# Kernel tuning notes

Measured on AMD Instinct MI355X. Metric: run time of the kernel, lower is better.

## Reference

```python
import jax, jax.numpy as jnp
import numpy as np

D, H, N, BS = 3072, 2048, 16, 512
MAX_LATENT_VAR = 0.1


def setup_inputs() -> dict:
    key = jax.random.key(0)
    ks = jax.random.split(key, 12)
    s = 0.02
    return {
        "x": jax.random.normal(ks[0], (BS, D), dtype=jnp.float32),
        "eps": jax.random.normal(ks[1], (1, BS, N), dtype=jnp.float32),
        "enc_W1": jax.random.normal(ks[2], (D, H), dtype=jnp.float32) * s,
        "enc_b1": jnp.zeros((H,), dtype=jnp.float32),
        "enc_Wmu": jax.random.normal(ks[3], (H, N), dtype=jnp.float32) * s,
        "enc_bmu": jnp.zeros((N,), dtype=jnp.float32),
        "enc_Wls": jax.random.normal(ks[4], (H, 1), dtype=jnp.float32) * s,
        "enc_bls": jnp.zeros((1,), dtype=jnp.float32),
        "dec_W1": jax.random.normal(ks[5], (N, H), dtype=jnp.float32) * 0.1,
        "dec_b1": jnp.zeros((H,), dtype=jnp.float32),
        "dec_W2": jax.random.normal(ks[6], (H, D), dtype=jnp.float32) * s,
        "dec_b2": jnp.zeros((D,), dtype=jnp.float32),
    }


def reference(x, eps, enc_W1, enc_b1, enc_Wmu, enc_bmu, enc_Wls, enc_bls,
              dec_W1, dec_b1, dec_W2, dec_b2):
    bs, Dd = x.shape
    n = dec_W1.shape[0]

    def dec(z):  # smooth 2-layer MLP decoder (supports nested autodiff)
        return jnp.tanh(z @ dec_W1 + dec_b1) @ dec_W2 + dec_b2

    # encoder.forward_with_sigma
    h = jnp.tanh(x @ enc_W1 + enc_b1)
    z_star = h @ enc_Wmu + enc_bmu                      # (bs, n)
    sigma = jnp.exp(h @ enc_Wls + enc_bls)[:, 0]        # (bs,)

    # per-sample Jacobian of decoder: (bs, D, n)
    J = jax.vmap(jax.jacfwd(dec))(z_star)

    # per-sample Hessian of f(z) = stop_grad(d) . d,  d = (x - dec(z)) / sigma
    def f_hess(z, xi, sg):
        d = (xi - dec(z)) / sg
        return jnp.dot(jax.lax.stop_gradient(d), d)
    hess = jax.vmap(jax.hessian(f_hess), in_axes=(0, 0, 0))(z_star, x, sigma)  # (bs,n,n)

    eye = jnp.eye(n, dtype=x.dtype)
    Prec = jnp.einsum('bdi,bdj->bij', J, J) / (sigma ** 2)[:, None, None] + eye + hess

    eigvals = jnp.linalg.eigvalsh(Prec)                 # ascending, (bs, n)
    eigmin = eigvals[:, 0]
    delta = 1.0 / MAX_LATENT_VAR - eigmin               # (bs,)
    Prec = Prec + eye * delta[:, None, None]
    eigvals = eigvals + delta[:, None]

    # upper-triangular Cholesky: U^T U = Prec
    U = jnp.swapaxes(jnp.linalg.cholesky(Prec), -1, -2)  # (bs, n, n)

    def solve1(u, e):  # solve U y = e
        return jax.scipy.linalg.solve_triangular(u, e[:, None], lower=False)[:, 0]
    z_off = jax.vmap(jax.vmap(solve1, in_axes=(0, 0)), in_axes=(None, 0))(U, eps)  # (ne,bs,n)
    z_sample = z_star[None] + z_off

    n_eval = eps.shape[0]
    recon = dec(z_sample.reshape(-1, n)).reshape(n_eval, bs, Dd)
    recon_loss = ((recon - x[None]) ** 2).sum(axis=2).mean(axis=0) / (2.0 * sigma ** 2)
    latent_energy = (z_star ** 2).sum(axis=1) / 2.0 + (1.0 / eigvals).sum(axis=1) / 2.0
    logdet_loss = jnp.log(eigvals).sum(axis=1) / 2.0
    sigma_loss = Dd * jnp.log(sigma)
    neg_log_prob = (recon_loss + latent_energy + logdet_loss + sigma_loss) / Dd
    return (neg_log_prob, recon_loss, latent_energy, logdet_loss, sigma)
```

## Files before the change

kernel.cpp:

```cpp
#include <hip/hip_runtime.h>
#include <hip/hip_bf16.h>
#include <math.h>

#define D_ 3072
#define H_ 2048
#define N_ 16
#define BS_ 512
#define NSL_ 8

typedef short s16x8 __attribute__((ext_vector_type(8)));
typedef float f32x4v __attribute__((ext_vector_type(4)));
typedef __hip_bfloat16 bf16;

__device__ __forceinline__ void gload_lds16(const void* g, void* l) {
    __builtin_amdgcn_global_load_lds((const __attribute__((address_space(1))) void*)g,
                                     (__attribute__((address_space(3))) void*)l, 16, 0, 0);
}

__device__ __forceinline__ float bf2f(unsigned short u) {
    unsigned v = (unsigned)u << 16; float f; __builtin_memcpy(&f, &v, 4); return f;
}

__global__ __launch_bounds__(256) void mfma_nt_slab(
    const bf16* __restrict__ A, const bf16* __restrict__ Bt,
    float* __restrict__ C, int M, int N, int K, int KC)
{
    __shared__ __align__(16) bf16 As[128 * 32];
    __shared__ __align__(16) bf16 Bs[128 * 32];
    const int tid = threadIdx.x;
    const int w = tid >> 6, l = tid & 63;
    const int wr = w >> 1, wc = w & 1;
    const int m0 = blockIdx.y * 128, n0 = blockIdx.x * 128;
    const int kbeg = blockIdx.z * KC;
    float* Cz = C + (size_t)blockIdx.z * M * N;

    f32x4v acc[4][4];
    #pragma unroll
    for (int a = 0; a < 4; ++a)
        #pragma unroll
        for (int b = 0; b < 4; ++b) acc[a][b] = (f32x4v){0.f, 0.f, 0.f, 0.f};

    const int srow = l >> 2;
    const int scol = (l & 3) * 8;

    for (int k0 = kbeg; k0 < kbeg + KC; k0 += 32) {
        #pragma unroll
        for (int q = 0; q < 2; ++q) {
            int r0 = w * 32 + q * 16;
            gload_lds16(&A[(size_t)(m0 + r0 + srow) * K + k0 + scol], &As[r0 * 32]);
            gload_lds16(&Bt[(size_t)(n0 + r0 + srow) * K + k0 + scol], &Bs[r0 * 32]);
        }
        __syncthreads();
        s16x8 af[4], bfr[4];
        #pragma unroll
        for (int mf = 0; mf < 4; ++mf)
            af[mf] = *(const s16x8*)&As[(wr * 64 + mf * 16 + (l & 15)) * 32 + (l >> 4) * 8];
        #pragma unroll
        for (int nf = 0; nf < 4; ++nf)
            bfr[nf] = *(const s16x8*)&Bs[(wc * 64 + nf * 16 + (l & 15)) * 32 + (l >> 4) * 8];
        #pragma unroll
        for (int mf = 0; mf < 4; ++mf)
            #pragma unroll
            for (int nf = 0; nf < 4; ++nf)
                acc[mf][nf] = __builtin_amdgcn_mfma_f32_16x16x32_bf16(af[mf], bfr[nf], acc[mf][nf], 0, 0, 0);
        __syncthreads();
    }

    #pragma unroll
    for (int mf = 0; mf < 4; ++mf)
        #pragma unroll
        for (int nf = 0; nf < 4; ++nf) {
            int n = n0 + wc * 64 + nf * 16 + (l & 15);
            #pragma unroll
            for (int r = 0; r < 4; ++r) {
                int m = m0 + wr * 64 + mf * 16 + (l >> 4) * 4 + r;
                Cz[(size_t)m * N + n] = acc[mf][nf][r];
            }
        }
}

__global__ __launch_bounds__(256) void mfma_nt_sk(
    const bf16* __restrict__ A, const bf16* __restrict__ Bt,
    float* __restrict__ C, int M, int N, int K, int KC)
{
    __shared__ __align__(16) bf16 As[128 * 32];
    __shared__ __align__(16) bf16 Bs[128 * 32];
    const int tid = threadIdx.x;
    const int w = tid >> 6, l = tid & 63;
    const int wr = w >> 1, wc = w & 1;
    const int m0 = blockIdx.y * 128, n0 = blockIdx.x * 128;
    const int kbeg = blockIdx.z * KC;

    f32x4v acc[4][4];
    #pragma unroll
    for (int a = 0; a < 4; ++a)
        #pragma unroll
        for (int b = 0; b < 4; ++b) acc[a][b] = (f32x4v){0.f, 0.f, 0.f, 0.f};

    const int srow = l >> 2;
    const int scol = (l & 3) * 8;

    for (int k0 = kbeg; k0 < kbeg + KC; k0 += 32) {
        #pragma unroll
        for (int q = 0; q < 2; ++q) {
            int r0 = w * 32 + q * 16;
            gload_lds16(&A[(size_t)(m0 + r0 + srow) * K + k0 + scol], &As[r0 * 32]);
            gload_lds16(&Bt[(size_t)(n0 + r0 + srow) * K + k0 + scol], &Bs[r0 * 32]);
        }
        __syncthreads();
        s16x8 af[4], bfr[4];
        #pragma unroll
        for (int mf = 0; mf < 4; ++mf)
            af[mf] = *(const s16x8*)&As[(wr * 64 + mf * 16 + (l & 15)) * 32 + (l >> 4) * 8];
        #pragma unroll
        for (int nf = 0; nf < 4; ++nf)
            bfr[nf] = *(const s16x8*)&Bs[(wc * 64 + nf * 16 + (l & 15)) * 32 + (l >> 4) * 8];
        #pragma unroll
        for (int mf = 0; mf < 4; ++mf)
            #pragma unroll
            for (int nf = 0; nf < 4; ++nf)
                acc[mf][nf] = __builtin_amdgcn_mfma_f32_16x16x32_bf16(af[mf], bfr[nf], acc[mf][nf], 0, 0, 0);
        __syncthreads();
    }

    #pragma unroll
    for (int mf = 0; mf < 4; ++mf)
        #pragma unroll
        for (int nf = 0; nf < 4; ++nf) {
            int n = n0 + wc * 64 + nf * 16 + (l & 15);
            #pragma unroll
            for (int r = 0; r < 4; ++r) {
                int m = m0 + wr * 64 + mf * 16 + (l >> 4) * 4 + r;
                atomicAdd(&C[(size_t)m * N + n], acc[mf][nf][r]);
            }
        }
}

__global__ __launch_bounds__(256) void ep_ebf(const float* __restrict__ C8,
    const float* __restrict__ bias, const float* __restrict__ X,
    bf16* __restrict__ Eout, int MN, int N)
{
    const size_t SL = (size_t)MN;
    int base = (blockIdx.x * 256 + threadIdx.x) * 8;
    if (base < MN) {
        float v[8] = {0.f, 0.f, 0.f, 0.f, 0.f, 0.f, 0.f, 0.f};
        #pragma unroll
        for (int s = 0; s < NSL_; ++s) {
            float4 c0 = *(const float4*)&C8[s * SL + base];
            float4 c1 = *(const float4*)&C8[s * SL + base + 4];
            v[0] += c0.x; v[1] += c0.y; v[2] += c0.z; v[3] += c0.w;
            v[4] += c1.x; v[5] += c1.y; v[6] += c1.z; v[7] += c1.w;
        }
        float4 x0 = *(const float4*)&X[base];
        float4 x1 = *(const float4*)&X[base + 4];
        int n = base % N;
        float4 b0 = *(const float4*)&bias[n];
        float4 b1 = *(const float4*)&bias[n + 4];
        union { s16x8 vv; bf16 e[8]; } u;
        u.e[0] = __float2bfloat16(x0.x - (v[0] + b0.x));
        u.e[1] = __float2bfloat16(x0.y - (v[1] + b0.y));
        u.e[2] = __float2bfloat16(x0.z - (v[2] + b0.z));
        u.e[3] = __float2bfloat16(x0.w - (v[3] + b0.w));
        u.e[4] = __float2bfloat16(x1.x - (v[4] + b1.x));
        u.e[5] = __float2bfloat16(x1.y - (v[5] + b1.y));
        u.e[6] = __float2bfloat16(x1.z - (v[6] + b1.z));
        u.e[7] = __float2bfloat16(x1.w - (v[7] + b1.w));
        *(s16x8*)&Eout[base] = u.vv;
    }
}

__global__ __launch_bounds__(256) void ep_recon_fin(const float* __restrict__ C8,
    const float* __restrict__ bias, const float* __restrict__ X,
    const float* __restrict__ sigma, const float* __restrict__ lsig, float* __restrict__ d_out)
{
    const size_t SL = (size_t)BS_ * D_;
    int m = blockIdx.x;
    float s = 0.f;
    for (int n = threadIdx.x * 4; n < D_; n += 1024) {
        size_t i = (size_t)m * D_ + n;
        float4 acc4 = (float4){0.f, 0.f, 0.f, 0.f};
        #pragma unroll
        for (int sl = 0; sl < NSL_; ++sl) {
            float4 c = *(const float4*)&C8[sl * SL + i];
            acc4.x += c.x; acc4.y += c.y; acc4.z += c.z; acc4.w += c.w;
        }
        float4 bb = *(const float4*)&bias[n];
        float4 xx = *(const float4*)&X[i];
        float v0 = acc4.x + bb.x - xx.x;
        float v1 = acc4.y + bb.y - xx.y;
        float v2 = acc4.z + bb.z - xx.z;
        float v3 = acc4.w + bb.w - xx.w;
        s += v0 * v0 + v1 * v1 + v2 * v2 + v3 * v3;
    }
    __shared__ float red[4];
    int wid = threadIdx.x >> 6, lane = threadIdx.x & 63;
    #pragma unroll
    for (int off = 32; off; off >>= 1) s += __shfl_xor(s, off);
    if (lane == 0) red[wid] = s;
    __syncthreads();
    if (threadIdx.x == 0) {
        float tot = red[0] + red[1] + red[2] + red[3];
        float sg = sigma[m];
        float rl = tot / (2.0f * sg * sg);
        float le = d_out[2 * 512 + m];
        float ld = d_out[3 * 512 + m];
        d_out[m] = (rl + le + ld) / 3072.0f + lsig[m];
        d_out[512 + m] = rl;
    }
}

__global__ __launch_bounds__(256) void jtj_fused(
    const bf16* __restrict__ Vt, const bf16* __restrict__ W2t,
    float* __restrict__ S, int Mb, int b0)
{
    __shared__ union {
        struct { __align__(16) bf16 As[3][128 * 32]; __align__(16) bf16 Bs[3][128 * 32]; } s;
        __align__(16) bf16 J[128 * 136];
    } u;
    const int tid = threadIdx.x;
    const int w = tid >> 6, l = tid & 63;
    const int wr = w >> 1, wc = w & 1;

    int mb, nbk;
    if ((Mb & 7) == 0) {
        int lin = blockIdx.y * 24 + blockIdx.x;
        int xcd = lin & 7, idx = lin >> 3;
        int mchunk = Mb >> 3;
        mb = xcd * mchunk + idx / 24;
        nbk = idx % 24;
    } else { mb = blockIdx.y; nbk = blockIdx.x; }
    const int m0 = mb * 128, n0 = nbk * 128;

    f32x4v acc[4][4];
    #pragma unroll
    for (int a = 0; a < 4; ++a)
        #pragma unroll
        for (int b = 0; b < 4; ++b) acc[a][b] = (f32x4v){0.f, 0.f, 0.f, 0.f};

    const int strow = tid >> 2;
    const int scb = (((tid & 3) ^ ((tid >> 3) & 3)) << 4);

    auto STAGE = [&](int kt, int bi) {
        const char* a0 = (const char*)Vt  + ((size_t)(m0 + strow) * H_ + kt * 32) * 2 + scb;
        const char* b0p = (const char*)W2t + ((size_t)(n0 + strow) * H_ + kt * 32) * 2 + scb;
        char* la = (char*)u.s.As[bi] + w * 1024;
        char* lb = (char*)u.s.Bs[bi] + w * 1024;
        gload_lds16(a0, la);
        gload_lds16(a0 + (size_t)64 * H_ * 2, la + 4096);
        gload_lds16(b0p, lb);
        gload_lds16(b0p + (size_t)64 * H_ * 2, lb + 4096);
    };

    STAGE(0, 0);
    STAGE(1, 1);

    const int rdcb = (((l >> 4) ^ ((l >> 1) & 3)) << 4);

    for (int kt = 0; kt < H_ / 32; ++kt) {
        __builtin_amdgcn_sched_barrier(0);
        if (kt == H_ / 32 - 1) asm volatile("s_waitcnt vmcnt(0)" ::: "memory");
        else                   asm volatile("s_waitcnt vmcnt(4)" ::: "memory");
        __builtin_amdgcn_s_barrier();
        __builtin_amdgcn_sched_barrier(0);
        const int cur = kt % 3;
        const char* Ab = (const char*)u.s.As[cur];
        const char* Bb = (const char*)u.s.Bs[cur];
        s16x8 af[4], bfr[4];
        #pragma unroll
        for (int mf = 0; mf < 4; ++mf)
            af[mf] = *(const s16x8*)(Ab + (wr * 64 + mf * 16 + (l & 15)) * 64 + rdcb);
        #pragma unroll
        for (int nf = 0; nf < 4; ++nf)
            bfr[nf] = *(const s16x8*)(Bb + (wc * 64 + nf * 16 + (l & 15)) * 64 + rdcb);
        if (kt + 2 < H_ / 32) STAGE(kt + 2, (kt + 2) % 3);
        #pragma unroll
        for (int mf = 0; mf < 4; ++mf)
            #pragma unroll
            for (int nf = 0; nf < 4; ++nf)
                acc[mf][nf] = __builtin_amdgcn_mfma_f32_16x16x32_bf16(af[mf], bfr[nf], acc[mf][nf], 0, 0, 0);
    }

    __syncthreads();
    #pragma unroll
    for (int mf = 0; mf < 4; ++mf) {
        int rbase = wr * 64 + mf * 16 + (l >> 4) * 4;
        #pragma unroll
        for (int nf = 0; nf < 4; ++nf) {
            int col = wc * 64 + nf * 16 + (l & 15);
            #pragma unroll
            for (int r = 0; r < 4; ++r)
                u.J[(rbase + r) * 136 + col] = __float2bfloat16(acc[mf][nf][r]);
        }
    }
    __syncthreads();

    #pragma unroll
    for (int t2 = 0; t2 < 2; ++t2) {
        int bl = w * 2 + t2;
        f32x4v sp = (f32x4v){0.f, 0.f, 0.f, 0.f};
        #pragma unroll
        for (int kq = 0; kq < 4; ++kq) {
            s16x8 fr = *(const s16x8*)&u.J[(bl * 16 + (l & 15)) * 136 + kq * 32 + (l >> 4) * 8];
            sp = __builtin_amdgcn_mfma_f32_16x16x32_bf16(fr, fr, sp, 0, 0, 0);
        }
        int bglob = b0 + mb * 8 + bl;
        #pragma unroll
        for (int r = 0; r < 4; ++r)
            atomicAdd(&S[(size_t)bglob * 256 + ((l >> 4) * 4 + r) * 16 + (l & 15)], sp[r]);
    }
}

__global__ __launch_bounds__(256) void prep_all(
    const float* __restrict__ x, const float* __restrict__ enc_W1,
    const float* __restrict__ dec_W2, const float* __restrict__ dec_W1,
    bf16* __restrict__ x_bf, bf16* __restrict__ eW1t,
    bf16* __restrict__ W2t, bf16* __restrict__ W2b, bf16* __restrict__ W1b,
    float* __restrict__ zero_region)
{
    __shared__ float tile[64][65];
    const int blk = blockIdx.x;
    const int tid = threadIdx.x;
    if (blk < 768) {
        int i = blk * 256 + tid;
        const float4* p = (const float4*)x + (size_t)i * 2;
        float4 a = p[0], b = p[1];
        union { s16x8 v; bf16 e[8]; } u;
        u.e[0] = __float2bfloat16(a.x); u.e[1] = __float2bfloat16(a.y);
        u.e[2] = __float2bfloat16(a.z); u.e[3] = __float2bfloat16(a.w);
        u.e[4] = __float2bfloat16(b.x); u.e[5] = __float2bfloat16(b.y);
        u.e[6] = __float2bfloat16(b.z); u.e[7] = __float2bfloat16(b.w);
        *(s16x8*)&x_bf[(size_t)i * 8] = u.v;
    } else if (blk < 768 + 1536) {
        int bid = blk - 768;
        int r0 = (bid % 48) * 64, c0 = (bid / 48) * 64;
        int tx = tid & 63, ty = tid >> 6;
        #pragma unroll
        for (int k = 0; k < 16; ++k) {
            int rr = ty * 16 + k;
            tile[rr][tx] = enc_W1[(size_t)(r0 + rr) * H_ + c0 + tx];
        }
        __syncthreads();
        #pragma unroll
        for (int k = 0; k < 16; ++k) {
            int cc = ty * 16 + k;
            eW1t[(size_t)(c0 + cc) * D_ + r0 + tx] = __float2bfloat16(tile[tx][cc]);
        }
    } else if (blk < 768 + 3072) {
        int bid = blk - 768 - 1536;
        int r0 = (bid % 32) * 64, c0 = (bid / 32) * 64;
        int tx = tid & 63, ty = tid >> 6;
        #pragma unroll
        for (int k = 0; k < 16; ++k) {
            int rr = ty * 16 + k;
            float v = dec_W2[(size_t)(r0 + rr) * D_ + c0 + tx];
            tile[rr][tx] = v;
            W2b[(size_t)(r0 + rr) * D_ + c0 + tx] = __float2bfloat16(v);
        }
        __syncthreads();
        #pragma unroll
        for (int k = 0; k < 16; ++k) {
            int cc = ty * 16 + k;
            W2t[(size_t)(c0 + cc) * H_ + r0 + tx] = __float2bfloat16(tile[tx][cc]);
        }
    } else if (blk < 768 + 3072 + 16) {
        int i = (blk - 768 - 3072) * 256 + tid;
        if (i < N_ * H_ / 8) {
            const float4* p = (const float4*)dec_W1 + (size_t)i * 2;
            float4 a = p[0], b = p[1];
            union { s16x8 v; bf16 e[8]; } u;
            u.e[0] = __float2bfloat16(a.x); u.e[1] = __float2bfloat16(a.y);
            u.e[2] = __float2bfloat16(a.z); u.e[3] = __float2bfloat16(a.w);
            u.e[4] = __float2bfloat16(b.x); u.e[5] = __float2bfloat16(b.y);
            u.e[6] = __float2bfloat16(b.z); u.e[7] = __float2bfloat16(b.w);
            *(s16x8*)&W1b[(size_t)i * 8] = u.v;
        }
    } else {
        int i = (blk - 768 - 3072 - 16) * 256 + tid;
        *(float4*)&zero_region[(size_t)i * 4] = (float4){0.f, 0.f, 0.f, 0.f};
    }
}

__global__ __launch_bounds__(256) void zsig_t_kernel(const float* __restrict__ Ch8,
    const float* __restrict__ enc_b1, const float* __restrict__ Wmu, const float* __restrict__ bmu,
    const float* __restrict__ Wls, const float* __restrict__ bls,
    const float* __restrict__ dW1, const float* __restrict__ db1,
    float* __restrict__ z_star, float* __restrict__ lsig, float* __restrict__ sigma,
    float* __restrict__ t, bf16* __restrict__ tb, bf16* __restrict__ Vt)
{
    const int b = blockIdx.x, tid = threadIdx.x;
    const size_t SL = (size_t)BS_ * H_;
    float acc[17];
    #pragma unroll
    for (int i = 0; i < 17; ++i) acc[i] = 0.f;
    for (int hh = tid; hh < H_; hh += 256) {
        size_t idx = (size_t)b * H_ + hh;
        float c = 0.f;
        #pragma unroll
        for (int s = 0; s < NSL_; ++s) c += Ch8[s * SL + idx];
        float hv = tanhf(c + enc_b1[hh]);
        const float* wr = &Wmu[(size_t)hh * 16];
        #pragma unroll
        for (int i = 0; i < 16; ++i) acc[i] += hv * wr[i];
        acc[16] += hv * Wls[hh];
    }
    __shared__ float red[17][4];
    __shared__ float zs[16];
    __shared__ float us[H_];
    const int wid = tid >> 6, lane = tid & 63;
    #pragma unroll
    for (int i = 0; i < 17; ++i) {
        float v = acc[i];
        #pragma unroll
        for (int off = 32; off; off >>= 1) v += __shfl_xor(v, off);
        if (lane == 0) red[i][wid] = v;
    }
    __syncthreads();
    if (tid < 17) {
        float v = red[tid][0] + red[tid][1] + red[tid][2] + red[tid][3];
        if (tid < 16) { float z = v + bmu[tid]; zs[tid] = z; z_star[(size_t)b * 16 + tid] = z; }
        else { float ls = v + bls[0]; lsig[b] = ls; sigma[b] = expf(ls); }
    }
    __syncthreads();
    for (int hh = tid; hh < H_; hh += 256) {
        float a = db1[hh];
        #pragma unroll
        for (int i = 0; i < 16; ++i) a += zs[i] * dW1[(size_t)i * H_ + hh];
        float tv = tanhf(a);
        t[(size_t)b * H_ + hh] = tv;
        tb[(size_t)b * H_ + hh] = __float2bfloat16(tv);
        us[hh] = 1.f - tv * tv;
    }
    if (Vt) {
        __syncthreads();
        size_t base = (size_t)b * 16 * H_;
        int hh = tid * 8;
        for (int i = 0; i < 16; ++i) {
            union { s16x8 v; bf16 e[8]; } pk;
            #pragma unroll
            for (int k = 0; k < 8; ++k)
                pk.e[k] = __float2bfloat16(us[hh + k] * dW1[(size_t)i * H_ + hh + k]);
            *(s16x8*)&Vt[base + (size_t)i * H_ + hh] = pk.v;
        }
    }
}

__global__ __launch_bounds__(256) void build_t(const float* __restrict__ z,
    const float* __restrict__ W1, const float* __restrict__ b1, bf16* __restrict__ tb)
{
    __shared__ float zs[16];
    int b = blockIdx.x, tid = threadIdx.x;
    if (tid < 16) zs[tid] = z[(size_t)b * 16 + tid];
    __syncthreads();
    for (int hh = tid; hh < H_; hh += 256) {
        float a = b1[hh];
        #pragma unroll
        for (int i = 0; i < 16; ++i) a += zs[i] * W1[(size_t)i * H_ + hh];
        tb[(size_t)b * H_ + hh] = __float2bfloat16(tanhf(a));
    }
}

__global__ __launch_bounds__(256) void build_vt(const float* __restrict__ t,
    const float* __restrict__ W1, bf16* __restrict__ Vt, int b0)
{
    int bl = blockIdx.x, b = b0 + bl, tid = threadIdx.x;
    __shared__ float u[H_];
    for (int hh = tid; hh < H_; hh += 256) {
        float tv = t[(size_t)b * H_ + hh];
        u[hh] = 1.f - tv * tv;
    }
    __syncthreads();
    size_t base = (size_t)bl * 16 * H_;
    int hh = tid * 8;
    for (int i = 0; i < 16; ++i) {
        union { s16x8 v; bf16 e[8]; } pk;
        #pragma unroll
        for (int k = 0; k < 8; ++k)
            pk.e[k] = __float2bfloat16(u[hh + k] * W1[(size_t)i * H_ + hh + k]);
        *(s16x8*)&Vt[base + (size_t)i * H_ + hh] = pk.v;
    }
}

__global__ __launch_bounds__(256) void solve_hess_kernel(
    const float* __restrict__ S, const float* __restrict__ t, const float* __restrict__ g,
    const bf16* __restrict__ W1b, const float* __restrict__ sigma,
    const float* __restrict__ z_star, const float* __restrict__ eps,
    float* __restrict__ z_sample, float* __restrict__ d_out)
{
    __shared__ float Sh[4][256];
    const int tid = threadIdx.x;
    {
        const int w = tid >> 6, l = tid & 63;
        const int b = blockIdx.x * 4 + w;
        const int row = l & 15, kq = (l >> 4) * 8;
        f32x4v sp = (f32x4v){0.f, 0.f, 0.f, 0.f};
        for (int k0 = 0; k0 < H_; k0 += 32) {
            int kk = k0 + kq;
            s16x8 wf = *(const s16x8*)&W1b[(size_t)row * H_ + kk];
            float4 t0 = *(const float4*)&t[(size_t)b * H_ + kk];
            float4 t1 = *(const float4*)&t[(size_t)b * H_ + kk + 4];
            float4 g0 = *(const float4*)&g[(size_t)b * H_ + kk];
            float4 g1 = *(const float4*)&g[(size_t)b * H_ + kk + 4];
            float wv[8];
            wv[0] = 2.f * g0.x * t0.x * (1.f - t0.x * t0.x);
            wv[1] = 2.f * g0.y * t0.y * (1.f - t0.y * t0.y);
            wv[2] = 2.f * g0.z * t0.z * (1.f - t0.z * t0.z);
            wv[3] = 2.f * g0.w * t0.w * (1.f - t0.w * t0.w);
            wv[4] = 2.f * g1.x * t1.x * (1.f - t1.x * t1.x);
            wv[5] = 2.f * g1.y * t1.y * (1.f - t1.y * t1.y);
            wv[6] = 2.f * g1.z * t1.z * (1.f - t1.z * t1.z);
            wv[7] = 2.f * g1.w * t1.w * (1.f - t1.w * t1.w);
            union { s16x8 v; bf16 e[8]; } af;
            #pragma unroll
            for (int e = 0; e < 8; ++e)
                af.e[e] = __float2bfloat16(wv[e] * bf2f((unsigned short)wf[e]));
            sp = __builtin_amdgcn_mfma_f32_16x16x32_bf16(af.v, wf, sp, 0, 0, 0);
        }
        #pragma unroll
        for (int r = 0; r < 4; ++r)
            Sh[w][((l >> 4) * 4 + r) * 16 + (l & 15)] = sp[r];
    }
    __syncthreads();
    if (tid >= 64) return;

    const int lane = tid;
    const int q = lane >> 4;
    const int j = lane & 15;
    const int b = blockIdx.x * 4 + q;

    const float sg = sigma[b];
    const float inv_s2 = 1.0f / (sg * sg);

    float a0[16], a[16];
    #pragma unroll
    for (int r = 0; r < 16; ++r) {
        a0[r] = (S[(size_t)b * 256 + r * 16 + j] + Sh[q][r * 16 + j]) * inv_s2 + ((r == j) ? 1.0f : 0.0f);
        a[r] = a0[r];
    }

    #pragma unroll
    for (int k = 0; k < 14; ++k) {
        float x[16];
        #pragma unroll
        for (int r = 0; r < 16; ++r) x[r] = __shfl(a[k], r, 16);
        float sig2 = 0.f;
        #pragma unroll
        for (int r = 0; r < 16; ++r) if (r > k + 1) sig2 += x[r] * x[r];
        float x0 = x[k + 1];
        float normx = sqrtf(sig2 + x0 * x0);
        float alpha = (x0 >= 0.f) ? -normx : normx;
        float v[16];
        #pragma unroll
        for (int r = 0; r < 16; ++r)
            v[r] = (r <= k) ? 0.f : ((r == k + 1) ? x0 - alpha : x[r]);
        float vtv = 0.f;
        #pragma unroll
        for (int r = 0; r < 16; ++r) vtv += v[r] * v[r];
        float beta = (vtv > 1e-28f) ? 2.0f / vtv : 0.f;
        float sj = 0.f;
        #pragma unroll
        for (int r = 0; r < 16; ++r) sj += a[r] * v[r];
        float av[16];
        #pragma unroll
        for (int r = 0; r < 16; ++r) av[r] = __shfl(sj, r, 16);
        float vtav = 0.f;
        #pragma unroll
        for (int r = 0; r < 16; ++r) vtav += v[r] * av[r];
        float c = 0.5f * beta * vtav;
        float wv[16];
        #pragma unroll
        for (int r = 0; r < 16; ++r) wv[r] = beta * (av[r] - c * v[r]);
        float vj = (j <= k) ? 0.f : ((j == k + 1) ? a[k] - alpha : a[k]);
        float wj = beta * (sj - c * vj);
        #pragma unroll
        for (int r = 0; r < 16; ++r) a[r] -= v[r] * wj + wv[r] * vj;
    }

    float dg[16], eo[15];
    #pragma unroll
    for (int r = 0; r < 16; ++r) dg[r] = __shfl(a[r], r, 16);
    #pragma unroll
    for (int r = 0; r < 15; ++r) eo[r] = __shfl(a[r + 1], r, 16);

    float lo = 1e30f, hi = 1e30f;
    #pragma unroll
    for (int r = 0; r < 16; ++r) {
        float rad = ((r > 0) ? fabsf(eo[r - 1]) : 0.f) + ((r < 15) ? fabsf(eo[r]) : 0.f);
        lo = fminf(lo, dg[r] - rad);
        hi = fminf(hi, dg[r]);
    }
    lo -= 1e-4f; hi += 1e-4f;

    #pragma unroll
    for (int pass = 0; pass < 5; ++pass) {
        float step = (hi - lo) * (1.0f / 17.0f);
        float s = lo + step * (float)(j + 1);
        float qq = dg[0] - s;
        int cnt = (qq < 0.f) ? 1 : 0;
        #pragma unroll
        for (int i = 1; i < 16; ++i) {
            float denom = (fabsf(qq) < 1e-30f) ? -1e-30f : qq;
            qq = dg[i] - s - eo[i - 1] * eo[i - 1] / denom;
            cnt += (qq < 0.f) ? 1 : 0;
        }
        unsigned long long bal = __ballot(cnt >= 1);
        unsigned grp = (unsigned)((bal >> (q * 16)) & 0xffffull);
        int f = grp ? (__ffs(grp) - 1) : 16;
        float nlo = lo + step * (float)f;
        float nhi = (f < 16) ? (lo + step * (float)(f + 1)) : hi;
        lo = nlo; hi = nhi;
    }
    const float lam_min = 0.5f * (lo + hi);
    const float delta = 10.0f - lam_min;

    float bm[16];
    #pragma unroll
    for (int r = 0; r < 16; ++r) bm[r] = a0[r] + ((r == j) ? delta : 0.f);

    float ldsum = 0.f;
    #pragma unroll
    for (int kk = 0; kk < 16; ++kk) {
        float ck[16];
        #pragma unroll
        for (int r = 0; r < 16; ++r) ck[r] = __shfl(bm[kk], r, 16);
        float dkk = sqrtf(fmaxf(ck[kk], 1e-30f));
        float inv = 1.0f / dkk;
        ldsum += logf(dkk);
        float lfull[16];
        #pragma unroll
        for (int r = 0; r < 16; ++r) lfull[r] = ck[r] * inv;
        float lj = bm[kk] * inv;
        if (j == kk) {
            #pragma unroll
            for (int r = 0; r < 16; ++r) bm[r] = (r >= kk) ? lfull[r] : 0.f;
        } else if (j > kk) {
            #pragma unroll
            for (int r = 0; r < 16; ++r)
                if (r > kk) bm[r] -= lfull[r] * lj;
        }
    }

    float w[16];
    #pragma unroll
    for (int r = 0; r < 16; ++r) w[r] = 0.f;
    #pragma unroll
    for (int i = 0; i < 16; ++i) {
        float row[16];
        #pragma unroll
        for (int kx = 0; kx < 16; ++kx) row[kx] = __shfl(bm[i], kx, 16);
        float sacc = 0.f;
        #pragma unroll
        for (int kx = 0; kx < 16; ++kx) if (kx < i) sacc += row[kx] * w[kx];
        float invd = 1.0f / row[i];
        float val = (i == j) ? invd : (-sacc * invd);
        w[i] = (i >= j) ? val : 0.f;
    }

    float tsum = 0.f;
    #pragma unroll
    for (int r = 0; r < 16; ++r) tsum += w[r] * w[r];
    float zv = z_star[(size_t)b * 16 + j];
    float ep = eps[(size_t)b * 16 + j];
    float epsv[16];
    #pragma unroll
    for (int r = 0; r < 16; ++r) epsv[r] = __shfl(ep, r, 16);
    float zoff = 0.f;
    #pragma unroll
    for (int r = 0; r < 16; ++r) zoff += w[r] * epsv[r];
    z_sample[(size_t)b * 16 + j] = zv + zoff;

    float zsq = zv * zv;
    #pragma unroll
    for (int off = 1; off < 16; off <<= 1) {
        tsum += __shfl_xor(tsum, off);
        zsq  += __shfl_xor(zsq, off);
    }
    if (j == 0) {
        d_out[2 * 512 + b] = 0.5f * zsq + 0.5f * tsum;
        d_out[3 * 512 + b] = ldsum;
        d_out[4 * 512 + b] = sg;
    }
}

extern "C" void kernel_launch(void* const* d_in, const int* in_sizes, int n_in,
                              void* d_out, int out_size, void* d_ws, size_t ws_size,
                              hipStream_t stream)
{
    const float* x       = (const float*)d_in[0];
    const float* eps     = (const float*)d_in[1];
    const float* enc_W1  = (const float*)d_in[2];
    const float* enc_b1  = (const float*)d_in[3];
    const float* enc_Wmu = (const float*)d_in[4];
    const float* enc_bmu = (const float*)d_in[5];
    const float* enc_Wls = (const float*)d_in[6];
    const float* enc_bls = (const float*)d_in[7];
    const float* dec_W1  = (const float*)d_in[8];
    const float* dec_b1  = (const float*)d_in[9];
    const float* dec_W2  = (const float*)d_in[10];
    const float* dec_b2  = (const float*)d_in[11];
    float* out = (float*)d_out;

    char* wsb = (char*)d_ws;
    size_t off = 0;
    auto alloc = [&](size_t bytes) -> void* {
        off = (off + 255) & ~(size_t)255;
        void* p = wsb + off;
        off += bytes;
        return p;
    };

    float* g    = (float*)alloc((size_t)BS_ * H_ * 4);
    float* S    = (float*)alloc((size_t)BS_ * 256 * 4);

    float* Ch8  = (float*)alloc((size_t)NSL_ * BS_ * H_ * 4);
    float* Cd8  = (float*)alloc((size_t)NSL_ * BS_ * D_ * 4);
    float* t    = (float*)alloc((size_t)BS_ * H_ * 4);
    float* z_st = (float*)alloc((size_t)BS_ * 16 * 4);
    float* lsig = (float*)alloc(BS_ * 4);
    float* sigm = (float*)alloc(BS_ * 4);
    float* z_sm = (float*)alloc((size_t)BS_ * 16 * 4);
    bf16* x_bf  = (bf16*)alloc((size_t)BS_ * D_ * 2);
    bf16* eW1t  = (bf16*)alloc((size_t)H_ * D_ * 2);
    bf16* W2b   = (bf16*)alloc((size_t)H_ * D_ * 2);
    bf16* W2t   = (bf16*)alloc((size_t)D_ * H_ * 2);
    bf16* W1b   = (bf16*)alloc((size_t)N_ * H_ * 2);
    bf16* t_bf  = (bf16*)alloc((size_t)BS_ * H_ * 2);
    bf16* e_bf  = (bf16*)alloc((size_t)BS_ * D_ * 2);
    bf16* t2b   = (bf16*)alloc((size_t)BS_ * H_ * 2);

    int nb = 0;
    size_t base_off = off;
    const int cand[3] = {512, 128, 32};
    bf16* Vt = nullptr;
    for (int ci = 0; ci < 3; ++ci) {
        off = base_off;
        int n = cand[ci];
        bf16* vt = (bf16*)alloc((size_t)n * 16 * H_ * 2);
        if (off <= ws_size) { nb = n; Vt = vt; break; }
    }
    if (nb == 0) return;
    bf16* Vt_full = (nb == 512) ? Vt : nullptr;

    prep_all<<<dim3(768 + 3072 + 16 + 1152), 256, 0, stream>>>(
        x, enc_W1, dec_W2, dec_W1, x_bf, eW1t, W2t, W2b, W1b, g);

    mfma_nt_slab<<<dim3(H_ / 128, BS_ / 128, NSL_), 256, 0, stream>>>(
        x_bf, eW1t, Ch8, BS_, H_, D_, D_ / NSL_);
    zsig_t_kernel<<<dim3(BS_), 256, 0, stream>>>(Ch8, enc_b1, enc_Wmu, enc_bmu, enc_Wls, enc_bls,
        dec_W1, dec_b1, z_st, lsig, sigm, t, t_bf, Vt_full);
    mfma_nt_slab<<<dim3(D_ / 128, BS_ / 128, NSL_), 256, 0, stream>>>(
        t_bf, W2t, Cd8, BS_, D_, H_, H_ / NSL_);
    ep_ebf<<<dim3(BS_ * D_ / 8 / 256), 256, 0, stream>>>(Cd8, dec_b2, x, e_bf, BS_ * D_, D_);
    mfma_nt_sk<<<dim3(H_ / 128, BS_ / 128, 4), 256, 0, stream>>>(
        e_bf, W2b, g, BS_, H_, D_, D_ / 4);

    if (Vt_full) {
        jtj_fused<<<dim3(D_ / 128, 512 * 16 / 128), 256, 0, stream>>>(
            Vt_full, W2t, S, 512 * 16 / 128, 0);
    } else {
        for (int b0 = 0; b0 < BS_; b0 += nb) {
            build_vt<<<dim3(nb), 256, 0, stream>>>(t, dec_W1, Vt, b0);
            jtj_fused<<<dim3(D_ / 128, nb * 16 / 128), 256, 0, stream>>>(
                Vt, W2t, S, nb * 16 / 128, b0);
        }
    }

    solve_hess_kernel<<<dim3(BS_ / 4), 256, 0, stream>>>(
        S, t, g, W1b, sigm, z_st, eps, z_sm, out);
    build_t<<<dim3(BS_), 256, 0, stream>>>(z_sm, dec_W1, dec_b1, t2b);
    mfma_nt_slab<<<dim3(D_ / 128, BS_ / 128, NSL_), 256, 0, stream>>>(
        t2b, W2t, Cd8, BS_, D_, H_, H_ / NSL_);
    ep_recon_fin<<<dim3(BS_), 256, 0, stream>>>(Cd8, dec_b2, x, sigm, lsig, out);
}
```

Baseline: 310.6 us.

## Build Jacobian A-operand on the fly inside JtJ GEMM instead of materializing Vt

Removes the materialized Vt tensor (512*16*2048 bf16) written by zsig_t_kernel or build_vt. The JtJ kernel now stages the fp32 tanh activations t and the bf16 dec_W1 tile into LDS and computes (1 - t^2) * W1 per fragment before each MFMA. This avoids a large global write and re-read of Vt, and the chunked fallback path for small workspaces goes away. In exchange it adds per-iteration ALU conversion work in the inner loop and reads t in fp32.

```diff
diff --git a/kernel.cpp b/kernel.cpp
--- a/kernel.cpp
+++ b/kernel.cpp
@@ -7,6 +7,7 @@
 #define N_ 16
 #define BS_ 512
 #define NSL_ 8
+#define NT_ (H_ / 32)
 
 typedef short s16x8 __attribute__((ext_vector_type(8)));
 typedef float f32x4v __attribute__((ext_vector_type(4)));
@@ -209,27 +210,29 @@
     }
 }
 
-__global__ __launch_bounds__(256) void jtj_fused(
-    const bf16* __restrict__ Vt, const bf16* __restrict__ W2t,
-    float* __restrict__ S, int Mb, int b0)
+__global__ __launch_bounds__(256) void jtj_tfly(
+    const float* __restrict__ t, const bf16* __restrict__ W1b,
+    const bf16* __restrict__ W2t, float* __restrict__ S, int Mb)
 {
     __shared__ union {
-        struct { __align__(16) bf16 As[3][128 * 32]; __align__(16) bf16 Bs[3][128 * 32]; } s;
+        struct {
+            __align__(16) bf16  W1s[3][16 * 32];
+            __align__(16) float Ts[3][8 * 32];
+            __align__(16) bf16  Bs[3][128 * 32];
+        } s;
         __align__(16) bf16 J[128 * 136];
     } u;
     const int tid = threadIdx.x;
     const int w = tid >> 6, l = tid & 63;
     const int wr = w >> 1, wc = w & 1;
 
-    int mb, nbk;
-    if ((Mb & 7) == 0) {
-        int lin = blockIdx.y * 24 + blockIdx.x;
-        int xcd = lin & 7, idx = lin >> 3;
-        int mchunk = Mb >> 3;
-        mb = xcd * mchunk + idx / 24;
-        nbk = idx % 24;
-    } else { mb = blockIdx.y; nbk = blockIdx.x; }
-    const int m0 = mb * 128, n0 = nbk * 128;
+    int lin = blockIdx.y * 24 + blockIdx.x;
+    int xcd = lin & 7, idx = lin >> 3;
+    int mchunk = Mb >> 3;
+    int mb = xcd * mchunk + idx / 24;
+    int nbk = idx % 24;
+    const int b0batch = mb * 8;
+    const int n0 = nbk * 128;
 
     f32x4v acc[4][4];
     #pragma unroll
@@ -241,14 +244,17 @@
     const int scb = (((tid & 3) ^ ((tid >> 3) & 3)) << 4);
 
     auto STAGE = [&](int kt, int bi) {
-        const char* a0 = (const char*)Vt  + ((size_t)(m0 + strow) * H_ + kt * 32) * 2 + scb;
         const char* b0p = (const char*)W2t + ((size_t)(n0 + strow) * H_ + kt * 32) * 2 + scb;
-        char* la = (char*)u.s.As[bi] + w * 1024;
         char* lb = (char*)u.s.Bs[bi] + w * 1024;
-        gload_lds16(a0, la);
-        gload_lds16(a0 + (size_t)64 * H_ * 2, la + 4096);
         gload_lds16(b0p, lb);
         gload_lds16(b0p + (size_t)64 * H_ * 2, lb + 4096);
+        if (w == 0) {
+            const char* src = (const char*)W1b + ((size_t)(l >> 2) * H_ + kt * 32 + (l & 3) * 8) * 2;
+            gload_lds16(src, (char*)u.s.W1s[bi]);
+        } else if (w == 1) {
+            const char* src = (const char*)t + ((size_t)(b0batch + (l >> 3)) * H_ + kt * 32 + (l & 7) * 4) * 4;
+            gload_lds16(src, (char*)u.s.Ts[bi]);
+        }
     };
 
     STAGE(0, 0);
@@ -256,23 +262,39 @@
 
     const int rdcb = (((l >> 4) ^ ((l >> 1) & 3)) << 4);
 
-    for (int kt = 0; kt < H_ / 32; ++kt) {
+    for (int kt = 0; kt < NT_; ++kt) {
         __builtin_amdgcn_sched_barrier(0);
-        if (kt == H_ / 32 - 1) asm volatile("s_waitcnt vmcnt(0)" ::: "memory");
-        else                   asm volatile("s_waitcnt vmcnt(4)" ::: "memory");
+        if (kt == NT_ - 1) asm volatile("s_waitcnt vmcnt(0)" ::: "memory");
+        else               asm volatile("s_waitcnt vmcnt(2)" ::: "memory");
         __builtin_amdgcn_s_barrier();
         __builtin_amdgcn_sched_barrier(0);
         const int cur = kt % 3;
-        const char* Ab = (const char*)u.s.As[cur];
-        const char* Bb = (const char*)u.s.Bs[cur];
-        s16x8 af[4], bfr[4];
-        #pragma unroll
-        for (int mf = 0; mf < 4; ++mf)
-            af[mf] = *(const s16x8*)(Ab + (wr * 64 + mf * 16 + (l & 15)) * 64 + rdcb);
+        s16x8 bfr[4];
         #pragma unroll
         for (int nf = 0; nf < 4; ++nf)
-            bfr[nf] = *(const s16x8*)(Bb + (wc * 64 + nf * 16 + (l & 15)) * 64 + rdcb);
-        if (kt + 2 < H_ / 32) STAGE(kt + 2, (kt + 2) % 3);
+            bfr[nf] = *(const s16x8*)((const char*)u.s.Bs[cur] + (wc * 64 + nf * 16 + (l & 15)) * 64 + rdcb);
+        s16x8 w1f = *(const s16x8*)((const char*)u.s.W1s[cur] + (l & 15) * 64 + (l >> 4) * 16);
+        float wv[8];
+        #pragma unroll
+        for (int j = 0; j < 8; ++j) wv[j] = bf2f((unsigned short)w1f[j]);
+        s16x8 af[4];
+        #pragma unroll
+        for (int mf = 0; mf < 4; ++mf) {
+            const float* tr = &u.s.Ts[cur][(wr * 4 + mf) * 32 + (l >> 4) * 8];
+            float4 t0 = *(const float4*)tr;
+            float4 t1 = *(const float4*)(tr + 4);
+            union { s16x8 v; bf16 e[8]; } pk;
+            pk.e[0] = __float2bfloat16((1.f - t0.x * t0.x) * wv[0]);
+            pk.e[1] = __float2bfloat16((1.f - t0.y * t0.y) * wv[1]);
+            pk.e[2] = __float2bfloat16((1.f - t0.z * t0.z) * wv[2]);
+            pk.e[3] = __float2bfloat16((1.f - t0.w * t0.w) * wv[3]);
+            pk.e[4] = __float2bfloat16((1.f - t1.x * t1.x) * wv[4]);
+            pk.e[5] = __float2bfloat16((1.f - t1.y * t1.y) * wv[5]);
+            pk.e[6] = __float2bfloat16((1.f - t1.z * t1.z) * wv[6]);
+            pk.e[7] = __float2bfloat16((1.f - t1.w * t1.w) * wv[7]);
+            af[mf] = pk.v;
+        }
+        if (kt + 2 < NT_) STAGE(kt + 2, (kt + 2) % 3);
         #pragma unroll
         for (int mf = 0; mf < 4; ++mf)
             #pragma unroll
@@ -303,7 +325,7 @@
             s16x8 fr = *(const s16x8*)&u.J[(bl * 16 + (l & 15)) * 136 + kq * 32 + (l >> 4) * 8];
             sp = __builtin_amdgcn_mfma_f32_16x16x32_bf16(fr, fr, sp, 0, 0, 0);
         }
-        int bglob = b0 + mb * 8 + bl;
+        int bglob = b0batch + bl;
         #pragma unroll
         for (int r = 0; r < 4; ++r)
             atomicAdd(&S[(size_t)bglob * 256 + ((l >> 4) * 4 + r) * 16 + (l & 15)], sp[r]);
@@ -385,7 +407,7 @@
     const float* __restrict__ Wls, const float* __restrict__ bls,
     const float* __restrict__ dW1, const float* __restrict__ db1,
     float* __restrict__ z_star, float* __restrict__ lsig, float* __restrict__ sigma,
-    float* __restrict__ t, bf16* __restrict__ tb, bf16* __restrict__ Vt)
+    float* __restrict__ t, bf16* __restrict__ tb)
 {
     const int b = blockIdx.x, tid = threadIdx.x;
     const size_t SL = (size_t)BS_ * H_;
@@ -405,7 +427,6 @@
     }
     __shared__ float red[17][4];
     __shared__ float zs[16];
-    __shared__ float us[H_];
     const int wid = tid >> 6, lane = tid & 63;
     #pragma unroll
     for (int i = 0; i < 17; ++i) {
@@ -428,19 +449,6 @@
         float tv = tanhf(a);
         t[(size_t)b * H_ + hh] = tv;
         tb[(size_t)b * H_ + hh] = __float2bfloat16(tv);
-        us[hh] = 1.f - tv * tv;
-    }
-    if (Vt) {
-        __syncthreads();
-        size_t base = (size_t)b * 16 * H_;
-        int hh = tid * 8;
-        for (int i = 0; i < 16; ++i) {
-            union { s16x8 v; bf16 e[8]; } pk;
-            #pragma unroll
-            for (int k = 0; k < 8; ++k)
-                pk.e[k] = __float2bfloat16(us[hh + k] * dW1[(size_t)i * H_ + hh + k]);
-            *(s16x8*)&Vt[base + (size_t)i * H_ + hh] = pk.v;
-        }
     }
 }
 
@@ -456,27 +464,6 @@
         #pragma unroll
         for (int i = 0; i < 16; ++i) a += zs[i] * W1[(size_t)i * H_ + hh];
         tb[(size_t)b * H_ + hh] = __float2bfloat16(tanhf(a));
-    }
-}
-
-__global__ __launch_bounds__(256) void build_vt(const float* __restrict__ t,
-    const float* __restrict__ W1, bf16* __restrict__ Vt, int b0)
-{
-    int bl = blockIdx.x, b = b0 + bl, tid = threadIdx.x;
-    __shared__ float u[H_];
-    for (int hh = tid; hh < H_; hh += 256) {
-        float tv = t[(size_t)b * H_ + hh];
-        u[hh] = 1.f - tv * tv;
-    }
-    __syncthreads();
-    size_t base = (size_t)bl * 16 * H_;
-    int hh = tid * 8;
-    for (int i = 0; i < 16; ++i) {
-        union { s16x8 v; bf16 e[8]; } pk;
-        #pragma unroll
-        for (int k = 0; k < 8; ++k)
-            pk.e[k] = __float2bfloat16(u[hh + k] * W1[(size_t)i * H_ + hh + k]);
-        *(s16x8*)&Vt[base + (size_t)i * H_ + hh] = pk.v;
     }
 }
 
@@ -726,19 +713,7 @@
     bf16* t_bf  = (bf16*)alloc((size_t)BS_ * H_ * 2);
     bf16* e_bf  = (bf16*)alloc((size_t)BS_ * D_ * 2);
     bf16* t2b   = (bf16*)alloc((size_t)BS_ * H_ * 2);
-
-    int nb = 0;
-    size_t base_off = off;
-    const int cand[3] = {512, 128, 32};
-    bf16* Vt = nullptr;
-    for (int ci = 0; ci < 3; ++ci) {
-        off = base_off;
-        int n = cand[ci];
-        bf16* vt = (bf16*)alloc((size_t)n * 16 * H_ * 2);
-        if (off <= ws_size) { nb = n; Vt = vt; break; }
-    }
-    if (nb == 0) return;
-    bf16* Vt_full = (nb == 512) ? Vt : nullptr;
+    if (off > ws_size) return;
 
     prep_all<<<dim3(768 + 3072 + 16 + 1152), 256, 0, stream>>>(
         x, enc_W1, dec_W2, dec_W1, x_bf, eW1t, W2t, W2b, W1b, g);
@@ -746,23 +721,14 @@
     mfma_nt_slab<<<dim3(H_ / 128, BS_ / 128, NSL_), 256, 0, stream>>>(
         x_bf, eW1t, Ch8, BS_, H_, D_, D_ / NSL_);
     zsig_t_kernel<<<dim3(BS_), 256, 0, stream>>>(Ch8, enc_b1, enc_Wmu, enc_bmu, enc_Wls, enc_bls,
-        dec_W1, dec_b1, z_st, lsig, sigm, t, t_bf, Vt_full);
+        dec_W1, dec_b1, z_st, lsig, sigm, t, t_bf);
     mfma_nt_slab<<<dim3(D_ / 128, BS_ / 128, NSL_), 256, 0, stream>>>(
         t_bf, W2t, Cd8, BS_, D_, H_, H_ / NSL_);
     ep_ebf<<<dim3(BS_ * D_ / 8 / 256), 256, 0, stream>>>(Cd8, dec_b2, x, e_bf, BS_ * D_, D_);
     mfma_nt_sk<<<dim3(H_ / 128, BS_ / 128, 4), 256, 0, stream>>>(
         e_bf, W2b, g, BS_, H_, D_, D_ / 4);
 
-    if (Vt_full) {
-        jtj_fused<<<dim3(D_ / 128, 512 * 16 / 128), 256, 0, stream>>>(
-            Vt_full, W2t, S, 512 * 16 / 128, 0);
-    } else {
-        for (int b0 = 0; b0 < BS_; b0 += nb) {
-            build_vt<<<dim3(nb), 256, 0, stream>>>(t, dec_W1, Vt, b0);
-            jtj_fused<<<dim3(D_ / 128, nb * 16 / 128), 256, 0, stream>>>(
-                Vt, W2t, S, nb * 16 / 128, b0);
-        }
-    }
+    jtj_tfly<<<dim3(24, 64), 256, 0, stream>>>(t, W1b, W2t, S, 64);
 
     solve_hess_kernel<<<dim3(BS_ / 4), 256, 0, stream>>>(
         S, t, g, W1b, sigm, z_st, eps, z_sm, out);
```

New measurement: 319.9 us. 1.03x slower.
